# Kernel optimization log

Hardware: AMD Instinct MI355X
Metric: run time of the kernel (lower is better)

## Reference

```python
import jax, jax.numpy as jnp
import numpy as np

N_SAMPLES = (16, 16)  # n_samples per layer (layer_specs)
N_MP = 2
N_HEAD = 4
BATCH = 512
N_NODES = 200000
MAX_DEG = 32
FEAT_DIM = 128
PREP_DIM = 128
HEAD_OUT = 64
ATT_HID = 128


def _agg_layer(x, nb, Wa1, wa2, Wx, Wn):
    # x: [m, d] self feats; nb: [m, S, d] neighbor feats
    # Wa1: [H, 2d, K], wa2: [H, K], Wx/Wn: [H, d, o]
    cat = jnp.concatenate([jnp.broadcast_to(x[:, None, :], nb.shape), nb], axis=-1)  # [m,S,2d]
    h = jnp.tanh(jnp.einsum('msd,hdk->mshk', cat, Wa1))          # [m,S,H,K]
    score = jnp.einsum('mshk,hk->mhs', h, wa2)                   # [m,H,S]
    alpha = jax.nn.softmax(score, axis=-1)
    agg = jnp.einsum('mhs,msd->mhd', alpha, nb)                  # [m,H,d]
    out = jax.nn.relu(jnp.einsum('md,hdo->mho', x, Wx) + jnp.einsum('mhd,hdo->mho', agg, Wn))
    return out.reshape(x.shape[0], -1)                           # concat heads -> [m, H*o]


def setup_inputs() -> dict:
    key = jax.random.key(0)
    ks = jax.random.split(key, 12)
    inp = {}
    inp['ids'] = jax.random.randint(ks[0], (BATCH,), 0, N_NODES, dtype=jnp.int32)
    inp['feats'] = jax.random.normal(ks[1], (N_NODES, FEAT_DIM), dtype=jnp.float32)
    inp['adjs'] = jax.random.randint(ks[2], (N_MP, N_NODES, MAX_DEG), 0, N_NODES, dtype=jnp.int32)
    inp['W_prep'] = jax.random.normal(ks[3], (FEAT_DIM, PREP_DIM), dtype=jnp.float32) / np.sqrt(FEAT_DIM)
    d0, d1 = PREP_DIM, N_HEAD * HEAD_OUT  # layer input dims: 128, 256
    inp['Watt1_0'] = jax.random.normal(ks[4], (N_MP, N_HEAD, 2 * d0, ATT_HID), dtype=jnp.float32) / np.sqrt(2 * d0)
    inp['watt2_0'] = jax.random.normal(ks[5], (N_MP, N_HEAD, ATT_HID), dtype=jnp.float32) / np.sqrt(ATT_HID)
    inp['Wx_0'] = jax.random.normal(ks[6], (N_MP, N_HEAD, d0, HEAD_OUT), dtype=jnp.float32) / np.sqrt(d0)
    inp['Wn_0'] = jax.random.normal(ks[7], (N_MP, N_HEAD, d0, HEAD_OUT), dtype=jnp.float32) / np.sqrt(d0)
    inp['Watt1_1'] = jax.random.normal(ks[8], (N_MP, N_HEAD, 2 * d1, ATT_HID), dtype=jnp.float32) / np.sqrt(2 * d1)
    inp['watt2_1'] = jax.random.normal(ks[9], (N_MP, N_HEAD, ATT_HID), dtype=jnp.float32) / np.sqrt(ATT_HID)
    inp['Wx_1'] = jax.random.normal(ks[10], (N_MP, N_HEAD, d1, HEAD_OUT), dtype=jnp.float32) / np.sqrt(d1)
    inp['Wn_1'] = jax.random.normal(ks[11], (N_MP, N_HEAD, d1, HEAD_OUT), dtype=jnp.float32) / np.sqrt(d1)
    return inp


def reference(ids, feats, adjs, W_prep, Watt1_0, watt2_0, Wx_0, Wn_0, Watt1_1, watt2_1, Wx_1, Wn_1):
    # eval mode (train=False): dropouts are identity
    init = feats[ids] @ W_prep  # prep(ids, feats[ids]) -> [B, 128]
    params = ((Watt1_0, watt2_0, Wx_0, Wn_0), (Watt1_1, watt2_1, Wx_1, Wn_1))
    outs = []
    for mp in range(N_MP):
        adj = adjs[mp]
        cur = ids
        all_feats = [init]
        # neighbor sampling + gather per layer (frontier: 512 -> 8192 -> 131072)
        for li, S in enumerate(N_SAMPLES):
            k = jax.random.fold_in(jax.random.key(42), mp * 16 + li)
            cols = jax.random.randint(k, (cur.shape[0], S), 0, MAX_DEG)
            cur = adj[cur[:, None], cols].reshape(-1)
            all_feats.append(feats[cur] @ W_prep)
        # depth aggregation: each layer collapses the frontier list by one level
        for li, (Wa1, wa2, Wx, Wn) in enumerate(params):
            new_feats = []
            for k_ in range(len(all_feats) - 1):
                x = all_feats[k_]
                nb = all_feats[k_ + 1].reshape(x.shape[0], N_SAMPLES[k_], -1)
                new_feats.append(_agg_layer(x, nb, Wa1[mp], wa2[mp], Wx[mp], Wn[mp]))
            all_feats = new_feats
        assert len(all_feats) == 1
        outs.append(all_feats[0])
    return jnp.stack(outs)  # [n_mp, B, n_head*head_out] = [2, 512, 256]
```

## Files before the change

kernel.cpp:

```cpp
#include <hip/hip_runtime.h>
#include <math.h>


typedef __attribute__((ext_vector_type(8))) short bf16x8;
typedef __attribute__((ext_vector_type(4))) float f32x4;

__device__ __forceinline__ float b2f(unsigned short u) {
  union { unsigned u; float f; } c; c.u = ((unsigned)u) << 16; return c.f;
}
__device__ __forceinline__ unsigned short f2b(float f) {
  union { float f; unsigned u; } c; c.f = f;
  return (unsigned short)((c.u + 0x7FFFu + ((c.u >> 16) & 1u)) >> 16);
}

__device__ __forceinline__ float fast_tanh(float x) {
  float y = x * 2.8853900817779268f;
  float z; asm("v_exp_f32 %0, %1" : "=v"(z) : "v"(y));
  float zp1 = z + 1.f;
  float w; asm("v_rcp_f32 %0, %1" : "=v"(w) : "v"(zp1));
  return fmaf(-2.f, w, 1.f);
}
__device__ __forceinline__ float fast_exp(float x) {
  float y = x * 1.4426950408889634f;
  float z; asm("v_exp_f32 %0, %1" : "=v"(z) : "v"(y));
  return z;
}

__host__ __device__ __forceinline__ void tf2x32(unsigned k0, unsigned k1,
                                                unsigned x0, unsigned x1,
                                                unsigned& o0, unsigned& o1) {
  const unsigned ks2 = k0 ^ k1 ^ 0x1BD11BDAu;
  unsigned v0 = x0 + k0, v1 = x1 + k1;
#define TFR(r) { v0 += v1; v1 = (v1 << (r)) | (v1 >> (32 - (r))); v1 ^= v0; }
  TFR(13) TFR(15) TFR(26) TFR(6)
  v0 += k1;  v1 += ks2 + 1u;
  TFR(17) TFR(29) TFR(16) TFR(24)
  v0 += ks2; v1 += k0 + 2u;
  TFR(13) TFR(15) TFR(26) TFR(6)
  v0 += k0;  v1 += k1 + 3u;
  TFR(17) TFR(29) TFR(16) TFR(24)
  v0 += k1;  v1 += ks2 + 4u;
  TFR(13) TFR(15) TFR(26) TFR(6)
  v0 += ks2; v1 += k0 + 5u;
#undef TFR
  o0 = v0; o1 = v1;
}

__global__ void frontier2_kernel(const int* __restrict__ adjs,
                                 const int* __restrict__ ids,
                                 int* __restrict__ nodes_all,
                                 unsigned a00, unsigned a01, unsigned b00, unsigned b01,
                                 unsigned a10, unsigned a11, unsigned b10, unsigned b11) {
  const int mp = blockIdx.z;
  const int* adj = adjs + (size_t)mp * 6400000;
  int* nodes = nodes_all + (size_t)mp * 139776;
  unsigned k0a = mp ? a10 : a00, k1a = mp ? a11 : a01;
  unsigned k0b = mp ? b10 : b00, k1b = mp ? b11 : b01;
  int i = blockIdx.x * 256 + threadIdx.x;
  int j = i >> 4;
  unsigned y0, y1;
  tf2x32(k0a, k1a, 0u, (unsigned)j, y0, y1);
  int col1 = (int)((y0 ^ y1) & 31u);
  int p0 = ids[j >> 4];
  int f1 = adj[(size_t)p0 * 32 + col1];
  tf2x32(k0b, k1b, 0u, (unsigned)i, y0, y1);
  int col2 = (int)((y0 ^ y1) & 31u);
  int f2 = adj[(size_t)f1 * 32 + col2];
  nodes[8704 + i] = f2;
  if ((i & 15) == 0) nodes[512 + j] = f1;
  if (i < 512) nodes[i] = ids[i];
}

__global__ void transcast_kernel(const float* __restrict__ Wp,
                                 const float* __restrict__ Wa1_0,
                                 const float* __restrict__ Wa1_1,
                                 const float* __restrict__ Wx_0,
                                 const float* __restrict__ Wn_0,
                                 const float* __restrict__ Wx_1,
                                 const float* __restrict__ Wn_1,
                                 unsigned short* __restrict__ Wpt) {
  int o = blockIdx.x * 256 + threadIdx.x;
  if (o >= 1196032) return;
  float v;
  if (o < 16384) {
    int k = o & 127, c = o >> 7;
    v = Wp[k * 128 + c];
  } else if (o < 278528) {
    int o2 = o - 16384;
    int k = o2 & 127, c = (o2 >> 7) & 127, h = (o2 >> 14) & 3,
        half = (o2 >> 16) & 1, mpi = o2 >> 17;
    v = Wa1_0[(((size_t)(mpi * 4 + h) * 256) + half * 128 + k) * 128 + c];
  } else if (o < 802816) {
    int o3 = o - 278528;
    int k = o3 & 255, c = (o3 >> 8) & 127, h = (o3 >> 15) & 3,
        half = (o3 >> 17) & 1, mpi = o3 >> 18;
    v = Wa1_1[(((size_t)(mpi * 4 + h) * 512) + half * 256 + k) * 128 + c];
  } else if (o < 868352) {
    int o4 = o - 802816;
    int k = o4 & 127, oo = (o4 >> 7) & 63, h = (o4 >> 13) & 3, mpi = o4 >> 15;
    v = Wx_0[(((size_t)(mpi * 4 + h) * 128) + k) * 64 + oo];
  } else if (o < 933888) {
    int o4 = o - 868352;
    int k = o4 & 127, oo = (o4 >> 7) & 63, h = (o4 >> 13) & 3, mpi = o4 >> 15;
    v = Wn_0[(((size_t)(mpi * 4 + h) * 128) + k) * 64 + oo];
  } else if (o < 1064960) {
    int o5 = o - 933888;
    int k = o5 & 255, oo = (o5 >> 8) & 63, h = (o5 >> 14) & 3, mpi = o5 >> 16;
    v = Wx_1[(((size_t)(mpi * 4 + h) * 256) + k) * 64 + oo];
  } else {
    int o5 = o - 1064960;
    int k = o5 & 255, oo = (o5 >> 8) & 63, h = (o5 >> 14) & 3, mpi = o5 >> 16;
    v = Wn_1[(((size_t)(mpi * 4 + h) * 256) + k) * 64 + oo];
  }
  Wpt[o] = f2b(v);
}

template <int MODE, bool A_F32, int NKS>
__global__ __launch_bounds__(256) void mfma_gemm(
    const void* __restrict__ Av, const int* __restrict__ gather,
    const unsigned short* __restrict__ WT, void* __restrict__ Cv,
    int ldc, int mclamp, int a_str, int g_str, int w_str, int c_str) {
  constexpr int K = NKS * 32;
  const int t = threadIdx.x;
  const int w = t >> 6, l = t & 63;
  const int lr = l & 15, lg = l >> 4;
  const int hb = blockIdx.y;
  const int mp = blockIdx.z;
  const int rbase = blockIdx.x * 128 + w * 32;

  const unsigned short* Wb = WT + (size_t)mp * w_str + (size_t)hb * 128 * K;
  f32x4 acc[2][8] = {};

  int arow[2];
#pragma unroll
  for (int mg = 0; mg < 2; ++mg) {
    int row = rbase + mg * 16 + lr;
    arow[mg] = gather ? gather[(size_t)mp * g_str + row] : min(row, mclamp);
  }
  const float* Af = (const float*)Av;
  const unsigned short* Ab = ((const unsigned short*)Av) + (size_t)mp * a_str;

#pragma unroll
  for (int ks = 0; ks < NKS; ++ks) {
    const int koff = ks * 32 + lg * 8;
    bf16x8 a[2], b[8];
#pragma unroll
    for (int mg = 0; mg < 2; ++mg) {
      if (A_F32) {
        const float* p = Af + (size_t)arow[mg] * K + koff;
        float4 v0 = *(const float4*)p;
        float4 v1 = *(const float4*)(p + 4);
        union { short s[8]; bf16x8 v; } u;
        u.s[0] = (short)f2b(v0.x); u.s[1] = (short)f2b(v0.y);
        u.s[2] = (short)f2b(v0.z); u.s[3] = (short)f2b(v0.w);
        u.s[4] = (short)f2b(v1.x); u.s[5] = (short)f2b(v1.y);
        u.s[6] = (short)f2b(v1.z); u.s[7] = (short)f2b(v1.w);
        a[mg] = u.v;
      } else {
        a[mg] = *(const bf16x8*)(Ab + (size_t)arow[mg] * K + koff);
      }
    }
#pragma unroll
    for (int f = 0; f < 8; ++f)
      b[f] = *(const bf16x8*)(Wb + (size_t)(f * 16 + lr) * K + koff);
#pragma unroll
    for (int mg = 0; mg < 2; ++mg)
#pragma unroll
      for (int f = 0; f < 8; ++f)
        acc[mg][f] = __builtin_amdgcn_mfma_f32_16x16x32_bf16(a[mg], b[f], acc[mg][f], 0, 0, 0);
  }

  if (MODE == 0) {
    unsigned short* Cb = ((unsigned short*)Cv) + (size_t)mp * c_str;
#pragma unroll
    for (int mg = 0; mg < 2; ++mg)
#pragma unroll
      for (int f = 0; f < 8; ++f)
#pragma unroll
        for (int r = 0; r < 4; ++r)
          Cb[(size_t)(rbase + mg * 16 + lg * 4 + r) * ldc + f * 16 + lr] =
              f2b(acc[mg][f][r]);
  } else {
    float* Cf = ((float*)Cv) + (size_t)mp * c_str;
#pragma unroll
    for (int mg = 0; mg < 2; ++mg)
#pragma unroll
      for (int f = 0; f < 8; ++f)
#pragma unroll
        for (int r = 0; r < 4; ++r)
          Cf[(size_t)(rbase + mg * 16 + lg * 4 + r) * ldc + hb * 128 + f * 16 + lr] =
              acc[mg][f][r];
  }
}

template <int NKS>
__global__ __launch_bounds__(256, 2) void aggsc_mfma(
    const unsigned short* __restrict__ NB, const int* __restrict__ gather,
    const float* __restrict__ Tb, const unsigned short* __restrict__ WTbot,
    const float* __restrict__ wa2, unsigned short* __restrict__ AG,
    int nb_str, int g_str, int t_str, int w_str, int wa2_str, int ag_str) {
  constexpr int K = NKS * 32;
  constexpr int KP = K + 8;
  const int t = threadIdx.x;
  const int w = t >> 6, l = t & 63;
  const int lr = l & 15, lg = l >> 4;
  const int mp = blockIdx.z;
  const int rbase = blockIdx.x * 64;

  __shared__ unsigned short NBs[64 * KP];
  __shared__ float alsh[4][4][16];

  const unsigned short* NBm = NB + (size_t)mp * nb_str;
  const int* gm = gather ? gather + (size_t)mp * g_str : nullptr;

#pragma unroll
  for (int q = 0; q < NKS; ++q) {
    int c = q * 256 + t;
    int row = c / (K / 8), kc = c % (K / 8);
    int src = gm ? gm[rbase + row] : (rbase + row);
    bf16x8 v = *(const bf16x8*)(NBm + (size_t)src * K + kc * 8);
    *(bf16x8*)(&NBs[row * KP + kc * 8]) = v;
  }
  __syncthreads();

  const unsigned short* Wb = WTbot + (size_t)mp * w_str + (size_t)w * 128 * K;
  float sc[4][4];
#pragma unroll
  for (int mg = 0; mg < 4; ++mg)
#pragma unroll
    for (int r = 0; r < 4; ++r) sc[mg][r] = 0.f;

#pragma unroll 1
  for (int half = 0; half < 2; ++half) {
    f32x4 acc[4][4] = {};
#pragma unroll
    for (int ks = 0; ks < NKS; ++ks) {
      const int koff = ks * 32 + lg * 8;
      bf16x8 a[4], b[4];
#pragma unroll
      for (int f = 0; f < 4; ++f)
        b[f] = *(const bf16x8*)(Wb + (size_t)(half * 64 + f * 16 + lr) * K + koff);
#pragma unroll
      for (int mg = 0; mg < 4; ++mg)
        a[mg] = *(const bf16x8*)(&NBs[(mg * 16 + lr) * KP + koff]);
#pragma unroll
      for (int mg = 0; mg < 4; ++mg)
#pragma unroll
        for (int f = 0; f < 4; ++f)
          acc[mg][f] = __builtin_amdgcn_mfma_f32_16x16x32_bf16(a[mg], b[f], acc[mg][f], 0, 0, 0);
    }
    float w2h[4];
#pragma unroll
    for (int f = 0; f < 4; ++f)
      w2h[f] = wa2[(size_t)mp * wa2_str + w * 128 + half * 64 + f * 16 + lr];
#pragma unroll
    for (int mg = 0; mg < 4; ++mg) {
      const int i = blockIdx.x * 4 + mg;
      float tvh[4];
#pragma unroll
      for (int f = 0; f < 4; ++f)
        tvh[f] = Tb[(size_t)mp * t_str + (size_t)i * 512 + w * 128 + half * 64 + f * 16 + lr];
#pragma unroll
      for (int r = 0; r < 4; ++r) {
        float s = 0.f;
#pragma unroll
        for (int f = 0; f < 4; ++f)
          s += fast_tanh(acc[mg][f][r] + tvh[f]) * w2h[f];
        sc[mg][r] += s;
      }
    }
  }

#pragma unroll
  for (int mg = 0; mg < 4; ++mg) {
    float s0 = sc[mg][0], s1 = sc[mg][1], s2 = sc[mg][2], s3 = sc[mg][3];
    s0 += __shfl_xor(s0, 1); s0 += __shfl_xor(s0, 2); s0 += __shfl_xor(s0, 4); s0 += __shfl_xor(s0, 8);
    s1 += __shfl_xor(s1, 1); s1 += __shfl_xor(s1, 2); s1 += __shfl_xor(s1, 4); s1 += __shfl_xor(s1, 8);
    s2 += __shfl_xor(s2, 1); s2 += __shfl_xor(s2, 2); s2 += __shfl_xor(s2, 4); s2 += __shfl_xor(s2, 8);
    s3 += __shfl_xor(s3, 1); s3 += __shfl_xor(s3, 2); s3 += __shfl_xor(s3, 4); s3 += __shfl_xor(s3, 8);
    float mx = fmaxf(fmaxf(s0, s1), fmaxf(s2, s3));
    mx = fmaxf(mx, __shfl_xor(mx, 16));
    mx = fmaxf(mx, __shfl_xor(mx, 32));
    float e0 = fast_exp(s0 - mx), e1 = fast_exp(s1 - mx);
    float e2 = fast_exp(s2 - mx), e3 = fast_exp(s3 - mx);
    float sum = e0 + e1 + e2 + e3;
    sum += __shfl_xor(sum, 16); sum += __shfl_xor(sum, 32);
    float inv = 1.f / sum;
    if (lr == 0) {
      alsh[w][mg][lg * 4 + 0] = e0 * inv;
      alsh[w][mg][lg * 4 + 1] = e1 * inv;
      alsh[w][mg][lg * 4 + 2] = e2 * inv;
      alsh[w][mg][lg * 4 + 3] = e3 * inv;
    }
  }

  constexpr int NCH = K >> 7;
#pragma unroll
  for (int mg = 0; mg < 4; ++mg) {
    const int i = blockIdx.x * 4 + mg;
    float al[16];
#pragma unroll
    for (int s = 0; s < 16; ++s) al[s] = alsh[w][mg][s];
#pragma unroll
    for (int c = 0; c < NCH; ++c) {
      const int d = l * 2 + c * 128;
      float a0 = 0.f, a1 = 0.f;
#pragma unroll
      for (int s = 0; s < 16; ++s) {
        unsigned v = *(const unsigned*)(&NBs[(mg * 16 + s) * KP + d]);
        a0 = fmaf(al[s], b2f((unsigned short)(v & 0xffffu)), a0);
        a1 = fmaf(al[s], b2f((unsigned short)(v >> 16)), a1);
      }
      unsigned o = (unsigned)f2b(a0) | ((unsigned)f2b(a1) << 16);
      *(unsigned*)(AG + (size_t)mp * ag_str + ((size_t)i * 4 + w) * K + d) = o;
    }
  }
}

template <int DX, bool OUTB>
__global__ __launch_bounds__(256) void outg_kernel(
    const unsigned short* __restrict__ Xb, const int* __restrict__ gatherX,
    const unsigned short* __restrict__ AG,
    const unsigned short* __restrict__ WXT, const unsigned short* __restrict__ WNT,
    void* __restrict__ outv,
    int x_str, int g_str, int ag_str, int w_str, int o_str) {
  const int t = threadIdx.x;
  const int w = t >> 6, l = t & 63;
  const int lr = l & 15, lg = l >> 4;
  const int hb = blockIdx.y;
  const int mp = blockIdx.z;
  const int rbase = blockIdx.x * 128 + w * 32;
  f32x4 acc[2][4] = {};
  constexpr int nks = DX >> 5;

  const unsigned short* Xm = Xb + (size_t)mp * x_str;
  const int* gm = gatherX ? gatherX + (size_t)mp * g_str : nullptr;
  const unsigned short* AGm = AG + (size_t)mp * ag_str;
  const unsigned short* WXm = WXT + (size_t)mp * w_str;
  const unsigned short* WNm = WNT + (size_t)mp * w_str;

  int xrow[2];
#pragma unroll
  for (int mg = 0; mg < 2; ++mg) {
    int row = rbase + mg * 16 + lr;
    xrow[mg] = gm ? gm[row] : row;
  }

#pragma unroll
  for (int ks = 0; ks < nks; ++ks) {
    const int koff = ks * 32 + lg * 8;
    bf16x8 a[2], b[4];
#pragma unroll
    for (int mg = 0; mg < 2; ++mg)
      a[mg] = *(const bf16x8*)(Xm + (size_t)xrow[mg] * DX + koff);
#pragma unroll
    for (int f = 0; f < 4; ++f)
      b[f] = *(const bf16x8*)(WXm + (size_t)(hb * 64 + f * 16 + lr) * DX + koff);
#pragma unroll
    for (int mg = 0; mg < 2; ++mg)
#pragma unroll
      for (int f = 0; f < 4; ++f)
        acc[mg][f] = __builtin_amdgcn_mfma_f32_16x16x32_bf16(a[mg], b[f], acc[mg][f], 0, 0, 0);
  }
#pragma unroll
  for (int ks = 0; ks < nks; ++ks) {
    const int koff = ks * 32 + lg * 8;
    bf16x8 a[2], b[4];
#pragma unroll
    for (int mg = 0; mg < 2; ++mg)
      a[mg] = *(const bf16x8*)(AGm + ((size_t)(rbase + mg * 16 + lr) * 4 + hb) * DX + koff);
#pragma unroll
    for (int f = 0; f < 4; ++f)
      b[f] = *(const bf16x8*)(WNm + (size_t)(hb * 64 + f * 16 + lr) * DX + koff);
#pragma unroll
    for (int mg = 0; mg < 2; ++mg)
#pragma unroll
      for (int f = 0; f < 4; ++f)
        acc[mg][f] = __builtin_amdgcn_mfma_f32_16x16x32_bf16(a[mg], b[f], acc[mg][f], 0, 0, 0);
  }

#pragma unroll
  for (int mg = 0; mg < 2; ++mg)
#pragma unroll
    for (int f = 0; f < 4; ++f)
#pragma unroll
      for (int r = 0; r < 4; ++r) {
        float v = fmaxf(acc[mg][f][r], 0.f);
        size_t idx = (size_t)mp * o_str +
                     (size_t)(rbase + mg * 16 + lg * 4 + r) * 256 + hb * 64 + f * 16 + lr;
        if (OUTB) ((unsigned short*)outv)[idx] = f2b(v);
        else      ((float*)outv)[idx] = v;
      }
}

extern "C" void kernel_launch(void* const* d_in, const int* in_sizes, int n_in,
                              void* d_out, int out_size, void* d_ws, size_t ws_size,
                              hipStream_t stream) {
  (void)in_sizes; (void)n_in; (void)out_size; (void)ws_size;
  const int*   ids   = (const int*)d_in[0];
  const float* feats = (const float*)d_in[1];
  const int*   adjs  = (const int*)d_in[2];
  const float* Wp    = (const float*)d_in[3];
  const float* Wa1_0 = (const float*)d_in[4];
  const float* wa2_0 = (const float*)d_in[5];
  const float* Wx_0  = (const float*)d_in[6];
  const float* Wn_0  = (const float*)d_in[7];
  const float* Wa1_1 = (const float*)d_in[8];
  const float* wa2_1 = (const float*)d_in[9];
  const float* Wx_1  = (const float*)d_in[10];
  const float* Wn_1  = (const float*)d_in[11];
  float* out = (float*)d_out;

  char* ws = (char*)d_ws;
  size_t off = 0;
  auto alloc = [&](size_t bytes) { char* p = ws + off; off += (bytes + 255) & ~(size_t)255; return p; };
  int*            nodes = (int*)alloc((size_t)2 * 139776 * 4);
  unsigned short* P_all = (unsigned short*)alloc((size_t)200064 * 128 * 2);
  float*          Tbig  = (float*)alloc((size_t)8192 * 512 * 4);
  float*          T2    = (float*)alloc((size_t)2 * 512 * 512 * 4);
  unsigned short* AGbig = (unsigned short*)alloc((size_t)8192 * 4 * 128 * 2);
  unsigned short* AG2   = (unsigned short*)alloc((size_t)2 * 512 * 4 * 256 * 2);
  unsigned short* NF1b  = (unsigned short*)alloc((size_t)2 * 8192 * 256 * 2);
  unsigned short* NF0b  = (unsigned short*)alloc((size_t)2 * 512 * 256 * 2);
  unsigned short* WB    = (unsigned short*)alloc((size_t)1196032 * 2);

  unsigned short* Wpt  = WB;
  unsigned short* WT0  = WB + 16384;
  unsigned short* WT1  = WB + 278528;
  unsigned short* WXT0 = WB + 802816;
  unsigned short* WNT0 = WB + 868352;
  unsigned short* WXT1 = WB + 933888;
  unsigned short* WNT1 = WB + 1064960;

  const int BIG = 1 << 30;

  unsigned key0[2][2], key1[2][2];
  for (int mp = 0; mp < 2; ++mp)
    for (int li = 0; li < 2; ++li) {
      unsigned K0, K1;
      tf2x32(0u, 42u, 0u, (unsigned)(mp * 16 + li), K0, K1);
      tf2x32(K0, K1, 0u, 1u, key0[mp][li], key1[mp][li]);
    }

  transcast_kernel<<<4672, 256, 0, stream>>>(Wp, Wa1_0, Wa1_1, Wx_0, Wn_0,
                                             Wx_1, Wn_1, WB);
  frontier2_kernel<<<dim3(512, 1, 2), 256, 0, stream>>>(
      adjs, ids, nodes,
      key0[0][0], key1[0][0], key0[0][1], key1[0][1],
      key0[1][0], key1[1][0], key0[1][1], key1[1][1]);

  mfma_gemm<0, true, 4><<<dim3(1563, 1, 1), 256, 0, stream>>>(
      feats, nullptr, Wpt, P_all, 128, 199999, 0, 0, 0, 0);

  for (int mp = 0; mp < 2; ++mp) {
    int* nmp = nodes + (size_t)mp * 139776;
    mfma_gemm<1, false, 4><<<dim3(64, 4, 1), 256, 0, stream>>>(
        P_all, nmp + 512, WT0 + (size_t)mp * 2 * 65536, Tbig, 512, BIG, 0, 0, 0, 0);
    aggsc_mfma<4><<<dim3(2048, 1, 1), 256, 0, stream>>>(
        P_all, nmp + 8704, Tbig, WT0 + ((size_t)mp * 2 + 1) * 65536,
        wa2_0 + (size_t)mp * 512, AGbig, 0, 0, 0, 0, 0, 0);
    outg_kernel<128, true><<<dim3(64, 4, 1), 256, 0, stream>>>(
        P_all, nmp + 512, AGbig, WXT0 + (size_t)mp * 32768, WNT0 + (size_t)mp * 32768,
        NF1b + (size_t)mp * 2097152, 0, 0, 0, 0, 0);
  }

  mfma_gemm<1, false, 4><<<dim3(4, 4, 2), 256, 0, stream>>>(
      P_all, nodes, WT0, T2, 512, BIG, 0, 139776, 131072, 262144);
  aggsc_mfma<4><<<dim3(128, 1, 2), 256, 0, stream>>>(
      P_all, nodes + 512, T2, WT0 + 65536, wa2_0, AG2,
      0, 139776, 262144, 131072, 512, 262144);
  outg_kernel<128, true><<<dim3(4, 4, 2), 256, 0, stream>>>(
      P_all, nodes, AG2, WXT0, WNT0, NF0b, 0, 139776, 262144, 32768, 131072);

  mfma_gemm<1, false, 8><<<dim3(4, 4, 2), 256, 0, stream>>>(
      NF0b, nullptr, WT1, T2, 512, 511, 131072, 0, 262144, 262144);
  aggsc_mfma<8><<<dim3(128, 1, 2), 256, 0, stream>>>(
      NF1b, nullptr, T2, WT1 + 131072, wa2_1, AG2,
      2097152, 0, 262144, 262144, 512, 524288);
  outg_kernel<256, false><<<dim3(4, 4, 2), 256, 0, stream>>>(
      NF0b, nullptr, AG2, WXT1, WNT1, out, 131072, 0, 524288, 65536, 131072);
}
```

Before: 298.9 us.

## Drop LDS staging in attention-score kernel; read neighbor rows directly from global

The aggsc kernel no longer copies the 64 gathered neighbor rows into shared memory. Each wave reads MFMA A-fragments and the aggregation operands straight from global memory, using row indices broadcast via shuffles. Softmax weights are passed by shuffles instead of an LDS array, which removes the block barrier and LDS traffic and may raise occupancy. The tanh input scale is folded into the attention weights during the transpose/cast, saving a multiply per element. The cost is that each wave now reloads the same rows from global/L2 (four waves, two halves), adding redundant memory traffic.

Result: slower. 340.3 us (+13.9%).

```diff
diff --git a/kernel.cpp b/kernel.cpp
--- a/kernel.cpp
+++ b/kernel.cpp
@@ -13,9 +13,8 @@
   return (unsigned short)((c.u + 0x7FFFu + ((c.u >> 16) & 1u)) >> 16);
 }
 
-__device__ __forceinline__ float fast_tanh(float x) {
-  float y = x * 2.8853900817779268f;
-  float z; asm("v_exp_f32 %0, %1" : "=v"(z) : "v"(y));
+__device__ __forceinline__ float fast_tanh_pre(float x) {
+  float z; asm("v_exp_f32 %0, %1" : "=v"(z) : "v"(x));
   float zp1 = z + 1.f;
   float w; asm("v_rcp_f32 %0, %1" : "=v"(w) : "v"(zp1));
   return fmaf(-2.f, w, 1.f);
@@ -79,6 +78,7 @@
                                  const float* __restrict__ Wx_1,
                                  const float* __restrict__ Wn_1,
                                  unsigned short* __restrict__ Wpt) {
+  const float TS = 2.8853900817779268f;
   int o = blockIdx.x * 256 + threadIdx.x;
   if (o >= 1196032) return;
   float v;
@@ -89,12 +89,12 @@
     int o2 = o - 16384;
     int k = o2 & 127, c = (o2 >> 7) & 127, h = (o2 >> 14) & 3,
         half = (o2 >> 16) & 1, mpi = o2 >> 17;
-    v = Wa1_0[(((size_t)(mpi * 4 + h) * 256) + half * 128 + k) * 128 + c];
+    v = TS * Wa1_0[(((size_t)(mpi * 4 + h) * 256) + half * 128 + k) * 128 + c];
   } else if (o < 802816) {
     int o3 = o - 278528;
     int k = o3 & 255, c = (o3 >> 8) & 127, h = (o3 >> 15) & 3,
         half = (o3 >> 17) & 1, mpi = o3 >> 18;
-    v = Wa1_1[(((size_t)(mpi * 4 + h) * 512) + half * 256 + k) * 128 + c];
+    v = TS * Wa1_1[(((size_t)(mpi * 4 + h) * 512) + half * 256 + k) * 128 + c];
   } else if (o < 868352) {
     int o4 = o - 802816;
     int k = o4 & 127, oo = (o4 >> 7) & 63, h = (o4 >> 13) & 3, mpi = o4 >> 15;
@@ -200,28 +200,15 @@
     const float* __restrict__ wa2, unsigned short* __restrict__ AG,
     int nb_str, int g_str, int t_str, int w_str, int wa2_str, int ag_str) {
   constexpr int K = NKS * 32;
-  constexpr int KP = K + 8;
   const int t = threadIdx.x;
   const int w = t >> 6, l = t & 63;
   const int lr = l & 15, lg = l >> 4;
   const int mp = blockIdx.z;
   const int rbase = blockIdx.x * 64;
 
-  __shared__ unsigned short NBs[64 * KP];
-  __shared__ float alsh[4][4][16];
-
   const unsigned short* NBm = NB + (size_t)mp * nb_str;
   const int* gm = gather ? gather + (size_t)mp * g_str : nullptr;
-
-#pragma unroll
-  for (int q = 0; q < NKS; ++q) {
-    int c = q * 256 + t;
-    int row = c / (K / 8), kc = c % (K / 8);
-    int src = gm ? gm[rbase + row] : (rbase + row);
-    bf16x8 v = *(const bf16x8*)(NBm + (size_t)src * K + kc * 8);
-    *(bf16x8*)(&NBs[row * KP + kc * 8]) = v;
-  }
-  __syncthreads();
+  const int myrow = gm ? gm[rbase + l] : (rbase + l);
 
   const unsigned short* Wb = WTbot + (size_t)mp * w_str + (size_t)w * 128 * K;
   float sc[4][4];
@@ -241,8 +228,10 @@
       for (int f = 0; f < 4; ++f)
         b[f] = *(const bf16x8*)(Wb + (size_t)(half * 64 + f * 16 + lr) * K + koff);
 #pragma unroll
-      for (int mg = 0; mg < 4; ++mg)
-        a[mg] = *(const bf16x8*)(&NBs[(mg * 16 + lr) * KP + koff]);
+      for (int mg = 0; mg < 4; ++mg) {
+        int src = __shfl(myrow, mg * 16 + lr);
+        a[mg] = *(const bf16x8*)(NBm + (size_t)src * K + koff);
+      }
 #pragma unroll
       for (int mg = 0; mg < 4; ++mg)
 #pragma unroll
@@ -265,14 +254,16 @@
         float s = 0.f;
 #pragma unroll
         for (int f = 0; f < 4; ++f)
-          s += fast_tanh(acc[mg][f][r] + tvh[f]) * w2h[f];
+          s += fast_tanh_pre(acc[mg][f][r] + tvh[f]) * w2h[f];
         sc[mg][r] += s;
       }
     }
   }
 
+  constexpr int NCH = K >> 7;
 #pragma unroll
   for (int mg = 0; mg < 4; ++mg) {
+    const int i = blockIdx.x * 4 + mg;
     float s0 = sc[mg][0], s1 = sc[mg][1], s2 = sc[mg][2], s3 = sc[mg][3];
     s0 += __shfl_xor(s0, 1); s0 += __shfl_xor(s0, 2); s0 += __shfl_xor(s0, 4); s0 += __shfl_xor(s0, 8);
     s1 += __shfl_xor(s1, 1); s1 += __shfl_xor(s1, 2); s1 += __shfl_xor(s1, 4); s1 += __shfl_xor(s1, 8);
@@ -286,30 +277,22 @@
     float sum = e0 + e1 + e2 + e3;
     sum += __shfl_xor(sum, 16); sum += __shfl_xor(sum, 32);
     float inv = 1.f / sum;
-    if (lr == 0) {
-      alsh[w][mg][lg * 4 + 0] = e0 * inv;
-      alsh[w][mg][lg * 4 + 1] = e1 * inv;
-      alsh[w][mg][lg * 4 + 2] = e2 * inv;
-      alsh[w][mg][lg * 4 + 3] = e3 * inv;
-    }
-  }
-
-  constexpr int NCH = K >> 7;
-#pragma unroll
-  for (int mg = 0; mg < 4; ++mg) {
-    const int i = blockIdx.x * 4 + mg;
-    float al[16];
-#pragma unroll
-    for (int s = 0; s < 16; ++s) al[s] = alsh[w][mg][s];
+    float ev0 = e0 * inv, ev1 = e1 * inv, ev2 = e2 * inv, ev3 = e3 * inv;
 #pragma unroll
     for (int c = 0; c < NCH; ++c) {
       const int d = l * 2 + c * 128;
       float a0 = 0.f, a1 = 0.f;
 #pragma unroll
       for (int s = 0; s < 16; ++s) {
-        unsigned v = *(const unsigned*)(&NBs[(mg * 16 + s) * KP + d]);
-        a0 = fmaf(al[s], b2f((unsigned short)(v & 0xffffu)), a0);
-        a1 = fmaf(al[s], b2f((unsigned short)(v >> 16)), a1);
+        float alv;
+        if ((s & 3) == 0)      alv = __shfl(ev0, (s >> 2) * 16);
+        else if ((s & 3) == 1) alv = __shfl(ev1, (s >> 2) * 16);
+        else if ((s & 3) == 2) alv = __shfl(ev2, (s >> 2) * 16);
+        else                   alv = __shfl(ev3, (s >> 2) * 16);
+        int src = __shfl(myrow, mg * 16 + s);
+        unsigned v = *(const unsigned*)(NBm + (size_t)src * K + d);
+        a0 = fmaf(alv, b2f((unsigned short)(v & 0xffffu)), a0);
+        a1 = fmaf(alv, b2f((unsigned short)(v >> 16)), a1);
       }
       unsigned o = (unsigned)f2b(a0) | ((unsigned)f2b(a1) << 16);
       *(unsigned*)(AG + (size_t)mp * ag_str + ((size_t)i * 4 + w) * K + d) = o;
```
